# Kernel optimization log

Measured on AMD Instinct MI355X. Metric: run time of the kernel, lower is better.

The kernel has to match this reference:

```python
import jax, jax.numpy as jnp
import numpy as np

NC = 80
CENTER_RADIUS = 2.5
TOPK = 10
BOX_W, CLS_W, OBJ_W = 7.5, 0.5, 1.0
ALPHA, GAMMA = 0.25, 2.0
EPS = 1e-7
BIG = 1e10


def _corners(b):
    x, y, w, h = b[..., 0], b[..., 1], b[..., 2], b[..., 3]
    return x - w / 2, y - h / 2, x + w / 2, y + h / 2


def _pairwise_iou(b1, b2):
    # b1: (N,4) xywh, b2: (G,4) xywh -> (N,G) plain IoU
    x11, y11, x12, y12 = [t[:, None] for t in _corners(b1)]
    x21, y21, x22, y22 = _corners(b2)
    inter = jnp.clip(jnp.minimum(x12, x22) - jnp.maximum(x11, x21), 0) * \
            jnp.clip(jnp.minimum(y12, y22) - jnp.maximum(y11, y21), 0)
    union = (b1[:, 2] * b1[:, 3])[:, None] + (b2[:, 2] * b2[:, 3])[None, :] - inter + EPS
    return inter / union


def _ciou(b1, b2):
    # aligned boxes (N,4),(N,4) xywh -> (N,) CIoU
    x11, y11, x12, y12 = _corners(b1)
    x21, y21, x22, y22 = _corners(b2)
    w1, h1 = b1[..., 2], b1[..., 3]
    w2, h2 = b2[..., 2], b2[..., 3]
    inter = jnp.clip(jnp.minimum(x12, x22) - jnp.maximum(x11, x21), 0) * \
            jnp.clip(jnp.minimum(y12, y22) - jnp.maximum(y11, y21), 0)
    union = w1 * h1 + w2 * h2 - inter + EPS
    iou = inter / union
    cw = jnp.maximum(x12, x22) - jnp.minimum(x11, x21)
    ch = jnp.maximum(y12, y22) - jnp.minimum(y11, y21)
    c2 = cw ** 2 + ch ** 2 + EPS
    rho2 = ((x11 + x12 - x21 - x22) ** 2 + (y11 + y12 - y21 - y22) ** 2) / 4
    v = (4.0 / jnp.pi ** 2) * (jnp.arctan(w2 / (h2 + EPS)) - jnp.arctan(w1 / (h1 + EPS))) ** 2
    alpha = jax.lax.stop_gradient(v / (v - iou + (1.0 + EPS)))
    return iou - (rho2 / c2 + v * alpha)


def _assign(pred_boxes, pred_scores, gt_boxes, gt_classes, anchor_centers):
    # SimOTA: returns fg mask (N,) bool and matched gt index per anchor (N,)
    N = pred_boxes.shape[0]
    G = gt_boxes.shape[0]
    d = jnp.sqrt(jnp.sum((anchor_centers[:, None, :] - gt_boxes[None, :, :2]) ** 2, -1))
    cand = (d < CENTER_RADIUS).any(axis=1)                      # (N,) center prior
    cand = jnp.where(cand.any(), cand, jnp.ones_like(cand))     # fallback: all anchors
    n_cand = cand.sum().astype(jnp.int32)
    iou = _pairwise_iou(pred_boxes, gt_boxes)                   # (N,G)
    iou = jnp.where(cand[:, None], iou, 0.0)                    # candidates only
    iou_cost = -jnp.log(iou + 1e-8)
    # cls cost: BCE-with-logits of sigmoid scores vs one-hot gt, summed over classes.
    # sum_c bce(s_c, y_c) = sum_c softplus(s_c) - s_{gt}; avoids (N,G,nc) tensor.
    sp_sum = jax.nn.softplus(pred_scores).sum(axis=1)           # (N,)
    cls_cost = sp_sum[:, None] - pred_scores[:, gt_classes]     # (N,G)
    cost = jnp.where(cand[:, None], iou_cost + 3.0 * cls_cost, BIG)
    # dynamic-k: k_j = clip(floor(sum_i iou[i,j]), 1, min(topk, n_cand))
    dyn_k = jnp.maximum(jnp.floor(iou.sum(axis=0)).astype(jnp.int32), 1)
    dyn_k = jnp.minimum(dyn_k, jnp.minimum(TOPK, n_cand))       # (G,)
    _, topk_idx = jax.lax.top_k(-cost.T, TOPK)                  # (G,TOPK) smallest-cost anchors
    keep = jnp.arange(TOPK)[None, :] < dyn_k[:, None]           # (G,TOPK)
    matching = jnp.zeros((G, N), dtype=bool).at[jnp.arange(G)[:, None], topk_idx].set(keep)
    matching = matching.T                                       # (N,G)
    # conflict resolution: anchors matched to >1 gt keep only min-cost gt
    count = matching.sum(axis=1)
    best = jnp.argmin(jnp.where(matching, cost, BIG), axis=1)
    matching = jnp.where((count > 1)[:, None], jax.nn.one_hot(best, G, dtype=bool), matching)
    fg = matching.any(axis=1)
    matched_gt = jnp.argmax(matching, axis=1)
    return fg, matched_gt


def _image_loss(pred, gt_boxes, gt_classes, anchor_centers):
    pb = pred[:, :4]
    pc = pred[:, 4:4 + NC]
    po = pred[:, -1]
    fg, mgt = _assign(pb, jax.nn.sigmoid(pc), gt_boxes, gt_classes, anchor_centers)
    fg_f = fg.astype(pred.dtype)
    # objectness: BCE-with-logits, mean over anchors
    obj = (jax.nn.softplus(po) - po * fg_f).mean()
    # box: CIoU on matched pairs (masked sum)
    tgt_boxes = gt_boxes[mgt]                                   # (N,4)
    box = jnp.sum((1.0 - _ciou(pb, tgt_boxes)) * fg_f)
    # cls: focal BCE on matched anchors
    tgt_cls = jax.nn.one_hot(gt_classes[mgt], NC, dtype=pred.dtype)
    bce = jax.nn.softplus(pc) - pc * tgt_cls
    p = jax.nn.sigmoid(pc)
    p_t = p * tgt_cls + (1 - p) * (1 - tgt_cls)
    cls = jnp.sum((ALPHA * (1 - p_t) ** GAMMA * bce).sum(axis=1) * fg_f)
    return box, cls, obj, fg_f.sum()


def setup_inputs() -> dict:
    B, N, M = 4, 33600, 100
    key = jax.random.key(0)
    ks = jax.random.split(key, 7)
    boxes_xy = jax.random.uniform(ks[0], (B, N, 2)) * 640.0
    boxes_wh = jax.random.uniform(ks[1], (B, N, 2)) * 100.0 + 10.0
    logits = jax.random.normal(ks[2], (B, N, NC + 1))
    pred = jnp.concatenate([boxes_xy, boxes_wh, logits], axis=-1)    # (B,N,85)
    gt_xy = jax.random.uniform(ks[3], (B, M, 2)) * 640.0
    gt_wh = jax.random.uniform(ks[4], (B, M, 2)) * 100.0 + 10.0
    gt_boxes = jnp.concatenate([gt_xy, gt_wh], axis=-1)              # (B,M,4), all valid (sum>0)
    gt_classes = jax.random.randint(ks[5], (B, M), 0, NC, dtype=jnp.int32)
    anchor_centers = jax.random.uniform(ks[6], (N, 2)) * 640.0
    return {"pred": pred, "gt_boxes": gt_boxes, "gt_classes": gt_classes,
            "anchor_centers": anchor_centers}


def reference(pred, gt_boxes, gt_classes, anchor_centers):
    box, cls, obj, npos = jax.vmap(_image_loss, in_axes=(0, 0, 0, None))(
        pred, gt_boxes, gt_classes, anchor_centers)
    n_pos = jnp.maximum(npos.sum(), 1.0)
    total = BOX_W * box.sum() / n_pos + CLS_W * cls.sum() / n_pos + OBJ_W * obj.sum()
    return total
```

## Files before the change

kernel.cpp:

```cpp
#include <hip/hip_runtime.h>
#include <math.h>

#define B_ 4
#define N_ 33600
#define G_ 100
#define NCLS 80
#define STRIDE 85
#define TK 10
#define K1BLK 132
#define K3BLK 525
#define CAP 2048
#define PADW (K1BLK * 256)

__device__ __forceinline__ float sigmoidf_(float x) {
    return 1.0f / (1.0f + expf(-x));
}
__device__ __forceinline__ float softplusf_(float x) {
    return fmaxf(x, 0.0f) + log1pf(expf(-fabsf(x)));
}
__device__ __forceinline__ float waveRedSum(float v) {
    #pragma unroll
    for (int off = 32; off; off >>= 1) v += __shfl_xor(v, off, 64);
    return v;
}

__global__ void k1_prep(const float* __restrict__ gtb,
                        const float* __restrict__ anc,
                        const float* __restrict__ pred,
                        int* __restrict__ cidx_pad,
                        float* __restrict__ spsum,
                        unsigned long long* __restrict__ bkey,
                        float* __restrict__ pobj,
                        int* __restrict__ bcount,
                        unsigned int* __restrict__ done)
{
    __shared__ float gcx[G_], gcy[G_];
    __shared__ int wsum[4];
    __shared__ float wsf[4];
    const int b = blockIdx.y;
    const int tid = threadIdx.x;
    const int lane = tid & 63, wid = tid >> 6;
    if (blockIdx.x == 0 && b == 0 && tid == 0) *done = 0u;
    if (tid < G_) {
        gcx[tid] = gtb[(b * G_ + tid) * 4 + 0];
        gcy[tid] = gtb[(b * G_ + tid) * 4 + 1];
    }
    __syncthreads();
    const int n = blockIdx.x * blockDim.x + tid;
    float so = 0.0f;
    int c = 0;
    if (n < N_) {
        const size_t a_ = (size_t)b * N_ + n;
        bkey[a_] = 0xFFFFFFFFFFFFFFFFull;
        so = softplusf_(pred[a_ * STRIDE + (STRIDE - 1)]);
        const float2 a = ((const float2*)anc)[n];
        #pragma unroll 10
        for (int g = 0; g < G_; ++g) {
            const float dx = a.x - gcx[g], dy = a.y - gcy[g];
            c |= (dx * dx + dy * dy < 6.25f) ? 1 : 0;
        }
        unsigned long long m = __ballot(c != 0);
        while (m) {
            const int src = (int)__ffsll(m) - 1;
            m &= (m - 1);
            const int an = __shfl(n, src, 64);
            const float* row = pred + ((size_t)b * N_ + an) * STRIDE + 4;
            float s = softplusf_(sigmoidf_(row[lane]));
            if (lane < NCLS - 64) s += softplusf_(sigmoidf_(row[64 + lane]));
            s = waveRedSum(s);
            if (lane == 0) spsum[(size_t)b * N_ + an] = s;
        }
    }
    int incl = c;
    #pragma unroll
    for (int off = 1; off < 64; off <<= 1) {
        const int t = __shfl_up(incl, off, 64);
        if (lane >= off) incl += t;
    }
    if (lane == 63) wsum[wid] = incl;
    const float sow = waveRedSum(so);
    if (lane == 0) wsf[wid] = sow;
    __syncthreads();
    int wbase = 0;
    for (int w = 0; w < wid; ++w) wbase += wsum[w];
    if (c) cidx_pad[(size_t)b * PADW + blockIdx.x * 256 + wbase + incl - 1] = n;
    if (tid == 0) {
        pobj[b * K1BLK + blockIdx.x] = wsf[0] + wsf[1] + wsf[2] + wsf[3];
        bcount[b * K1BLK + blockIdx.x] = wsum[0] + wsum[1] + wsum[2] + wsum[3];
    }
}

__global__ void __launch_bounds__(256)
k2_topk(const float* __restrict__ pred,
        const float* __restrict__ gtb,
        const int* __restrict__ gtc,
        const int* __restrict__ cidx_pad,
        const int* __restrict__ bcount,
        const float* __restrict__ spsum,
        unsigned long long* __restrict__ bkey)
{
    const int b = blockIdx.y, g = blockIdx.x;
    const int tid = threadIdx.x;
    const int lane = tid & 63, wid = tid >> 6;

    __shared__ int scan[256];
    __shared__ int clds[CAP];
    __shared__ unsigned long long warr[4][TK];
    __shared__ float iolds[4];

    const int myc = (tid < K1BLK) ? bcount[b * K1BLK + tid] : 0;
    scan[tid] = myc;
    __syncthreads();
    #pragma unroll
    for (int off = 1; off < 256; off <<= 1) {
        const int v = (tid >= off) ? scan[tid - off] : 0;
        __syncthreads();
        scan[tid] += v;
        __syncthreads();
    }
    const int cnt = scan[K1BLK - 1];
    const int allc = (cnt == 0) ? 1 : 0;
    const int count = allc ? N_ : cnt;
    const int ebase = (tid == 0) ? 0 : scan[tid - 1];

    const float* gb = gtb + (b * G_ + g) * 4;
    const float gxc = gb[0], gyc = gb[1], gw = gb[2], gh = gb[3];
    const float gx1 = gxc - gw * 0.5f, gy1 = gyc - gh * 0.5f;
    const float gx2 = gxc + gw * 0.5f, gy2 = gyc + gh * 0.5f;
    const float garea = gw * gh;
    const int cls = gtc[b * G_ + g];

    float kcost[TK];
    int   kid[TK];
    #pragma unroll
    for (int j = 0; j < TK; ++j) { kcost[j] = INFINITY; kid[j] = 0x7FFFFFFF; }
    float iousum = 0.0f;

    for (int lo = 0; lo < count; lo += CAP) {
        const int hi = (count < lo + CAP) ? count : (lo + CAP);
        if (!allc && tid < K1BLK && myc) {
            for (int j = 0; j < myc; ++j) {
                const int d = ebase + j;
                if (d >= lo && d < hi)
                    clds[d - lo] = cidx_pad[(size_t)b * PADW + tid * 256 + j];
            }
        }
        __syncthreads();
        for (int i = lo + tid; i < hi; i += 256) {
            int n;
            float sp;
            if (allc) {
                n = i;
                const float* pr0 = pred + (size_t)(b * N_ + n) * STRIDE;
                float s = 0.0f;
                for (int cc = 0; cc < NCLS; ++cc) s += softplusf_(sigmoidf_(pr0[4 + cc]));
                sp = s;
            } else {
                n = clds[i - lo];
                sp = spsum[(size_t)b * N_ + n];
            }
            const float* pr = pred + (size_t)(b * N_ + n) * STRIDE;
            const float px = pr[0], py = pr[1], pw = pr[2], ph = pr[3];
            const float x1 = px - pw * 0.5f, y1 = py - ph * 0.5f;
            const float x2 = px + pw * 0.5f, y2 = py + ph * 0.5f;
            const float iw = fmaxf(fminf(x2, gx2) - fmaxf(x1, gx1), 0.0f);
            const float ih = fmaxf(fminf(y2, gy2) - fmaxf(y1, gy1), 0.0f);
            const float inter = iw * ih;
            const float uni = pw * ph + garea - inter + 1e-7f;
            const float iou = inter / uni;
            iousum += iou;
            const float sgc = sigmoidf_(pr[4 + cls]);
            float c = -logf(iou + 1e-8f) + 3.0f * (sp - sgc);
            int   s = n;
            #pragma unroll
            for (int j = 0; j < TK; ++j) {
                const bool lt = (c < kcost[j]);
                const float tc = kcost[j]; const int ts = kid[j];
                if (lt) { kcost[j] = c; kid[j] = s; c = tc; s = ts; }
            }
        }
        __syncthreads();
    }

    const float ios = waveRedSum(iousum);
    if (lane == 0) iolds[wid] = ios;

    #pragma unroll
    for (int r = 0; r < TK; ++r) {
        const unsigned long long mykey =
            ((unsigned long long)__float_as_uint(kcost[0]) << 32) | (unsigned)kid[0];
        unsigned long long k2 = mykey;
        #pragma unroll
        for (int off = 32; off; off >>= 1) {
            const unsigned long long o = __shfl_xor(k2, off, 64);
            k2 = (o < k2) ? o : k2;
        }
        if (lane == 0) warr[wid][r] = k2;
        if (mykey == k2) {
            #pragma unroll
            for (int j = 0; j < TK - 1; ++j) { kcost[j] = kcost[j + 1]; kid[j] = kid[j + 1]; }
            kcost[TK - 1] = INFINITY; kid[TK - 1] = 0x7FFFFFFF;
        }
    }
    __syncthreads();

    if (wid == 0) {
        unsigned long long key = 0xFFFFFFFFFFFFFFFFull;
        if (lane < 4 * TK) key = warr[lane / TK][lane % TK];
        unsigned long long win[TK];
        #pragma unroll
        for (int r = 0; r < TK; ++r) {
            unsigned long long k2 = key;
            #pragma unroll
            for (int off = 32; off; off >>= 1) {
                const unsigned long long o = __shfl_xor(k2, off, 64);
                k2 = (o < k2) ? o : k2;
            }
            win[r] = k2;
            if (key == k2) key = 0xFFFFFFFFFFFFFFFFull;
        }
        const float total_iou = iolds[0] + iolds[1] + iolds[2] + iolds[3];
        const int kmax = (count < TK) ? count : TK;
        int dk = (int)floorf(total_iou);
        if (dk < 1) dk = 1;
        if (dk > kmax) dk = kmax;
        if (lane == 0) {
            #pragma unroll
            for (int r = 0; r < TK; ++r) {
                if (r < dk) {
                    const int n = (int)(unsigned)(win[r] & 0xFFFFFFFFull);
                    const unsigned cbits = (unsigned)(win[r] >> 32);
                    const unsigned long long key2 =
                        ((unsigned long long)cbits << 32) | (unsigned)g;
                    atomicMin(&bkey[(size_t)b * N_ + n], key2);
                }
            }
        }
    }
}

__global__ void k3_fg(const float* __restrict__ pred,
                      const float* __restrict__ gtb,
                      const int* __restrict__ gtc,
                      const unsigned long long* __restrict__ bkey,
                      const float* __restrict__ pobj,
                      float* __restrict__ pfg,
                      unsigned int* __restrict__ done,
                      float* __restrict__ out)
{
    const int tid = threadIdx.x;
    const unsigned i = blockIdx.x * blockDim.x + tid;
    const int lane = tid & 63, wid = tid >> 6;
    const unsigned long long key = bkey[i];
    const bool fg = (key != 0xFFFFFFFFFFFFFFFFull);
    float posum = 0.0f, box = 0.0f, clsacc = 0.0f, npos = 0.0f;

    unsigned long long m = __ballot(fg);
    while (m) {
        const int src = (int)__ffsll(m) - 1;
        m &= (m - 1);
        const unsigned ai = (unsigned)__shfl((int)i, src, 64);
        const int mg = __shfl((int)(unsigned)(key & 0xFFFFFFFFull), src, 64);
        const int b = (int)(ai / (unsigned)N_);
        const float* pr = pred + (size_t)ai * STRIDE;
        const int cg_ = gtc[b * G_ + mg];
        {
            const float x = pr[4 + lane];
            const float t = (lane == cg_) ? 1.0f : 0.0f;
            const float bce = softplusf_(x) - x * t;
            const float p = sigmoidf_(x);
            const float pt = t * p + (1.0f - t) * (1.0f - p);
            const float om = 1.0f - pt;
            clsacc += 0.25f * om * om * bce;
        }
        if (lane < NCLS - 64) {
            const float x = pr[4 + 64 + lane];
            const float t = ((64 + lane) == cg_) ? 1.0f : 0.0f;
            const float bce = softplusf_(x) - x * t;
            const float p = sigmoidf_(x);
            const float pt = t * p + (1.0f - t) * (1.0f - p);
            const float om = 1.0f - pt;
            clsacc += 0.25f * om * om * bce;
        }
        if (lane == 0) {
            npos += 1.0f;
            posum += pr[STRIDE - 1];
            const float* gb = gtb + (b * G_ + mg) * 4;
            const float px = pr[0], py = pr[1], pw = pr[2], ph = pr[3];
            const float gx = gb[0], gy = gb[1], gw = gb[2], gh = gb[3];
            const float x11 = px - pw * 0.5f, y11 = py - ph * 0.5f;
            const float x12 = px + pw * 0.5f, y12 = py + ph * 0.5f;
            const float x21 = gx - gw * 0.5f, y21 = gy - gh * 0.5f;
            const float x22 = gx + gw * 0.5f, y22 = gy + gh * 0.5f;
            const float iw = fmaxf(fminf(x12, x22) - fmaxf(x11, x21), 0.0f);
            const float ih = fmaxf(fminf(y12, y22) - fmaxf(y11, y21), 0.0f);
            const float inter = iw * ih;
            const float uni = pw * ph + gw * gh - inter + 1e-7f;
            const float iou = inter / uni;
            const float cw = fmaxf(x12, x22) - fminf(x11, x21);
            const float chh = fmaxf(y12, y22) - fminf(y11, y21);
            const float c2 = cw * cw + chh * chh + 1e-7f;
            const float ddx = x11 + x12 - x21 - x22;
            const float ddy = y11 + y12 - y21 - y22;
            const float rho2 = (ddx * ddx + ddy * ddy) * 0.25f;
            const float dv = atanf(gw / (gh + 1e-7f)) - atanf(pw / (ph + 1e-7f));
            const float v = (float)(4.0 / (M_PI * M_PI)) * dv * dv;
            const float alpha = v / (v - iou + 1.0f + 1e-7f);
            const float ciou = iou - (rho2 / c2 + v * alpha);
            box += 1.0f - ciou;
        }
    }

    posum = waveRedSum(posum);
    box = waveRedSum(box);
    clsacc = waveRedSum(clsacc);
    npos = waveRedSum(npos);
    __shared__ float ws[4][4];
    if (lane == 0) {
        ws[wid][0] = posum; ws[wid][1] = box;
        ws[wid][2] = clsacc; ws[wid][3] = npos;
    }
    __syncthreads();
    __shared__ int amlast;
    if (tid == 0) {
        float* p = pfg + (size_t)blockIdx.x * 4;
        #pragma unroll
        for (int k = 0; k < 4; ++k) {
            const float v = ws[0][k] + ws[1][k] + ws[2][k] + ws[3][k];
            __hip_atomic_store(&p[k], v, __ATOMIC_RELAXED, __HIP_MEMORY_SCOPE_AGENT);
        }
        const unsigned prev = __hip_atomic_fetch_add(done, 1u, __ATOMIC_ACQ_REL,
                                                     __HIP_MEMORY_SCOPE_AGENT);
        amlast = (prev == (unsigned)(K3BLK - 1)) ? 1 : 0;
    }
    __syncthreads();
    if (!amlast) return;

    float so = 0, sp = 0, sb = 0, sc = 0, sn = 0;
    for (int k = tid; k < B_ * K1BLK; k += 256) so += pobj[k];
    for (int k = tid; k < K3BLK; k += 256) {
        const float* p = pfg + (size_t)k * 4;
        sp += __hip_atomic_load(&p[0], __ATOMIC_RELAXED, __HIP_MEMORY_SCOPE_AGENT);
        sb += __hip_atomic_load(&p[1], __ATOMIC_RELAXED, __HIP_MEMORY_SCOPE_AGENT);
        sc += __hip_atomic_load(&p[2], __ATOMIC_RELAXED, __HIP_MEMORY_SCOPE_AGENT);
        sn += __hip_atomic_load(&p[3], __ATOMIC_RELAXED, __HIP_MEMORY_SCOPE_AGENT);
    }
    __shared__ float red[256];
    float in5[5] = {so, sp, sb, sc, sn};
    float res[5];
    #pragma unroll
    for (int k = 0; k < 5; ++k) {
        red[tid] = in5[k];
        __syncthreads();
        for (int s = 128; s > 0; s >>= 1) {
            if (tid < s) red[tid] += red[tid + s];
            __syncthreads();
        }
        res[k] = red[0];
        __syncthreads();
    }
    if (tid == 0) {
        const float obj_sum = res[0] - res[1];
        const float n_pos = fmaxf(res[4], 1.0f);
        out[0] = 7.5f * res[2] / n_pos
               + 0.5f * res[3] / n_pos
               + obj_sum / (float)N_;
    }
}

extern "C" void kernel_launch(void* const* d_in, const int* in_sizes, int n_in,
                              void* d_out, int out_size, void* d_ws, size_t ws_size,
                              hipStream_t stream)
{
    const float* pred = (const float*)d_in[0];
    const float* gtb  = (const float*)d_in[1];
    const int*   gtc  = (const int*)d_in[2];
    const float* anc  = (const float*)d_in[3];

    char* ws = (char*)d_ws;
    size_t off = 0;
    auto take = [&](size_t bytes) {
        size_t o = off;
        off += (bytes + 255) & ~(size_t)255;
        return o;
    };
    int*                cidx_pad = (int*)(ws + take((size_t)B_ * PADW * 4));
    unsigned long long* bkey     = (unsigned long long*)(ws + take((size_t)B_ * N_ * 8));
    float*              spsum    = (float*)(ws + take((size_t)B_ * N_ * 4));
    float*              pobj     = (float*)(ws + take((size_t)B_ * K1BLK * 4));
    int*                bcount   = (int*)(ws + take((size_t)B_ * K1BLK * 4));
    float*              pfg      = (float*)(ws + take((size_t)K3BLK * 4 * 4));
    unsigned int*       done     = (unsigned int*)(ws + take(4));

    dim3 g1(K1BLK, B_);
    k1_prep<<<g1, 256, 0, stream>>>(gtb, anc, pred, cidx_pad, spsum, bkey,
                                    pobj, bcount, done);
    dim3 g2(G_, B_);
    k2_topk<<<g2, 256, 0, stream>>>(pred, gtb, gtc, cidx_pad, bcount, spsum, bkey);
    k3_fg<<<K3BLK, 256, 0, stream>>>(pred, gtb, gtc, bkey, pobj, pfg, done,
                                     (float*)d_out);
}
```

Before: 41.52 us.

## Fuse foreground loss into top-k assignment kernel via atomicMin delta accounting

```diff
diff --git a/kernel.cpp b/kernel.cpp
--- a/kernel.cpp
+++ b/kernel.cpp
@@ -8,7 +8,7 @@
 #define STRIDE 85
 #define TK 10
 #define K1BLK 132
-#define K3BLK 525
+#define K2TOT (B_ * G_)
 #define CAP 2048
 #define PADW (K1BLK * 256)
 
@@ -32,6 +32,7 @@
                         unsigned long long* __restrict__ bkey,
                         float* __restrict__ pobj,
                         int* __restrict__ bcount,
+                        float* __restrict__ acc,
                         unsigned int* __restrict__ done)
 {
     __shared__ float gcx[G_], gcy[G_];
@@ -40,7 +41,10 @@
     const int b = blockIdx.y;
     const int tid = threadIdx.x;
     const int lane = tid & 63, wid = tid >> 6;
-    if (blockIdx.x == 0 && b == 0 && tid == 0) *done = 0u;
+    if (blockIdx.x == 0 && b == 0 && tid == 0) {
+        *done = 0u;
+        acc[0] = 0.0f; acc[1] = 0.0f; acc[2] = 0.0f; acc[3] = 0.0f;
+    }
     if (tid < G_) {
         gcx[tid] = gtb[(b * G_ + tid) * 4 + 0];
         gcy[tid] = gtb[(b * G_ + tid) * 4 + 1];
@@ -90,14 +94,78 @@
     }
 }
 
+struct Contrib { float cls, box, po; };
+__device__ __noinline__ Contrib contribEval(const float* __restrict__ pred,
+                                            const float* __restrict__ gtb,
+                                            const int* __restrict__ gtc,
+                                            int b, int n, int gg, int lane)
+{
+    Contrib c;
+    const float* pr = pred + (size_t)(b * N_ + n) * STRIDE;
+    const int cg_ = gtc[b * G_ + gg];
+    float cl;
+    {
+        const float x = pr[4 + lane];
+        const float t = (lane == cg_) ? 1.0f : 0.0f;
+        const float bce = softplusf_(x) - x * t;
+        const float p = sigmoidf_(x);
+        const float pt = t * p + (1.0f - t) * (1.0f - p);
+        const float om = 1.0f - pt;
+        cl = 0.25f * om * om * bce;
+    }
+    if (lane < NCLS - 64) {
+        const float x = pr[4 + 64 + lane];
+        const float t = ((64 + lane) == cg_) ? 1.0f : 0.0f;
+        const float bce = softplusf_(x) - x * t;
+        const float p = sigmoidf_(x);
+        const float pt = t * p + (1.0f - t) * (1.0f - p);
+        const float om = 1.0f - pt;
+        cl += 0.25f * om * om * bce;
+    }
+    c.cls = cl;
+    c.box = 0.0f;
+    c.po = 0.0f;
+    if (lane == 0) {
+        c.po = pr[STRIDE - 1];
+        const float* gb = gtb + (b * G_ + gg) * 4;
+        const float px = pr[0], py = pr[1], pw = pr[2], ph = pr[3];
+        const float gx = gb[0], gy = gb[1], gw = gb[2], gh = gb[3];
+        const float x11 = px - pw * 0.5f, y11 = py - ph * 0.5f;
+        const float x12 = px + pw * 0.5f, y12 = py + ph * 0.5f;
+        const float x21 = gx - gw * 0.5f, y21 = gy - gh * 0.5f;
+        const float x22 = gx + gw * 0.5f, y22 = gy + gh * 0.5f;
+        const float iw = fmaxf(fminf(x12, x22) - fmaxf(x11, x21), 0.0f);
+        const float ih = fmaxf(fminf(y12, y22) - fmaxf(y11, y21), 0.0f);
+        const float inter = iw * ih;
+        const float uni = pw * ph + gw * gh - inter + 1e-7f;
+        const float iou = inter / uni;
+        const float cw = fmaxf(x12, x22) - fminf(x11, x21);
+        const float chh = fmaxf(y12, y22) - fminf(y11, y21);
+        const float c2 = cw * cw + chh * chh + 1e-7f;
+        const float ddx = x11 + x12 - x21 - x22;
+        const float ddy = y11 + y12 - y21 - y22;
+        const float rho2 = (ddx * ddx + ddy * ddy) * 0.25f;
+        const float dv = atanf(gw / (gh + 1e-7f)) - atanf(pw / (ph + 1e-7f));
+        const float v = (float)(4.0 / (M_PI * M_PI)) * dv * dv;
+        const float alpha = v / (v - iou + 1.0f + 1e-7f);
+        const float ciou = iou - (rho2 / c2 + v * alpha);
+        c.box = 1.0f - ciou;
+    }
+    return c;
+}
+
 __global__ void __launch_bounds__(256)
-k2_topk(const float* __restrict__ pred,
-        const float* __restrict__ gtb,
-        const int* __restrict__ gtc,
-        const int* __restrict__ cidx_pad,
-        const int* __restrict__ bcount,
-        const float* __restrict__ spsum,
-        unsigned long long* __restrict__ bkey)
+k2_assign(const float* __restrict__ pred,
+          const float* __restrict__ gtb,
+          const int* __restrict__ gtc,
+          const int* __restrict__ cidx_pad,
+          const int* __restrict__ bcount,
+          const float* __restrict__ spsum,
+          unsigned long long* __restrict__ bkey,
+          const float* __restrict__ pobj,
+          float* __restrict__ acc,
+          unsigned int* __restrict__ done,
+          float* __restrict__ out)
 {
     const int b = blockIdx.y, g = blockIdx.x;
     const int tid = threadIdx.x;
@@ -107,6 +175,8 @@
     __shared__ int clds[CAP];
     __shared__ unsigned long long warr[4][TK];
     __shared__ float iolds[4];
+    __shared__ unsigned long long swin[TK];
+    __shared__ int sdk;
 
     const int myc = (tid < K1BLK) ? bcount[b * K1BLK + tid] : 0;
     scan[tid] = myc;
@@ -207,7 +277,6 @@
     if (wid == 0) {
         unsigned long long key = 0xFFFFFFFFFFFFFFFFull;
         if (lane < 4 * TK) key = warr[lane / TK][lane % TK];
-        unsigned long long win[TK];
         #pragma unroll
         for (int r = 0; r < TK; ++r) {
             unsigned long long k2 = key;
@@ -216,98 +285,40 @@
                 const unsigned long long o = __shfl_xor(k2, off, 64);
                 k2 = (o < k2) ? o : k2;
             }
-            win[r] = k2;
+            if (lane == 0) swin[r] = k2;
             if (key == k2) key = 0xFFFFFFFFFFFFFFFFull;
         }
-        const float total_iou = iolds[0] + iolds[1] + iolds[2] + iolds[3];
-        const int kmax = (count < TK) ? count : TK;
-        int dk = (int)floorf(total_iou);
-        if (dk < 1) dk = 1;
-        if (dk > kmax) dk = kmax;
         if (lane == 0) {
-            #pragma unroll
-            for (int r = 0; r < TK; ++r) {
-                if (r < dk) {
-                    const int n = (int)(unsigned)(win[r] & 0xFFFFFFFFull);
-                    const unsigned cbits = (unsigned)(win[r] >> 32);
-                    const unsigned long long key2 =
-                        ((unsigned long long)cbits << 32) | (unsigned)g;
-                    atomicMin(&bkey[(size_t)b * N_ + n], key2);
-                }
+            const float total_iou = iolds[0] + iolds[1] + iolds[2] + iolds[3];
+            const int kmax = (count < TK) ? count : TK;
+            int dk = (int)floorf(total_iou);
+            if (dk < 1) dk = 1;
+            if (dk > kmax) dk = kmax;
+            sdk = dk;
+        }
+    }
+    __syncthreads();
+
+    float clsacc = 0.0f, box = 0.0f, posum = 0.0f, npos = 0.0f;
+    const int dk = sdk;
+    for (int r = wid; r < dk; r += 4) {
+        const unsigned long long w = swin[r];
+        const int n = (int)(unsigned)(w & 0xFFFFFFFFull);
+        const unsigned long long mykey =
+            (w & 0xFFFFFFFF00000000ull) | (unsigned)g;
+        unsigned long long old = 0;
+        if (lane == 0) old = atomicMin(&bkey[(size_t)b * N_ + n], mykey);
+        old = __shfl(old, 0, 64);
+        if (mykey < old) {
+            const Contrib ca = contribEval(pred, gtb, gtc, b, n, g, lane);
+            clsacc += ca.cls; box += ca.box; posum += ca.po;
+            if (lane == 0) npos += 1.0f;
+            if (old != 0xFFFFFFFFFFFFFFFFull) {
+                const int og = (int)(unsigned)(old & 0xFFFFFFFFull);
+                const Contrib cs = contribEval(pred, gtb, gtc, b, n, og, lane);
+                clsacc -= cs.cls; box -= cs.box; posum -= cs.po;
+                if (lane == 0) npos -= 1.0f;
             }
-        }
-    }
-}
-
-__global__ void k3_fg(const float* __restrict__ pred,
-                      const float* __restrict__ gtb,
-                      const int* __restrict__ gtc,
-                      const unsigned long long* __restrict__ bkey,
-                      const float* __restrict__ pobj,
-                      float* __restrict__ pfg,
-                      unsigned int* __restrict__ done,
-                      float* __restrict__ out)
-{
-    const int tid = threadIdx.x;
-    const unsigned i = blockIdx.x * blockDim.x + tid;
-    const int lane = tid & 63, wid = tid >> 6;
-    const unsigned long long key = bkey[i];
-    const bool fg = (key != 0xFFFFFFFFFFFFFFFFull);
-    float posum = 0.0f, box = 0.0f, clsacc = 0.0f, npos = 0.0f;
-
-    unsigned long long m = __ballot(fg);
-    while (m) {
-        const int src = (int)__ffsll(m) - 1;
-        m &= (m - 1);
-        const unsigned ai = (unsigned)__shfl((int)i, src, 64);
-        const int mg = __shfl((int)(unsigned)(key & 0xFFFFFFFFull), src, 64);
-        const int b = (int)(ai / (unsigned)N_);
-        const float* pr = pred + (size_t)ai * STRIDE;
-        const int cg_ = gtc[b * G_ + mg];
-        {
-            const float x = pr[4 + lane];
-            const float t = (lane == cg_) ? 1.0f : 0.0f;
-            const float bce = softplusf_(x) - x * t;
-            const float p = sigmoidf_(x);
-            const float pt = t * p + (1.0f - t) * (1.0f - p);
-            const float om = 1.0f - pt;
-            clsacc += 0.25f * om * om * bce;
-        }
-        if (lane < NCLS - 64) {
-            const float x = pr[4 + 64 + lane];
-            const float t = ((64 + lane) == cg_) ? 1.0f : 0.0f;
-            const float bce = softplusf_(x) - x * t;
-            const float p = sigmoidf_(x);
-            const float pt = t * p + (1.0f - t) * (1.0f - p);
-            const float om = 1.0f - pt;
-            clsacc += 0.25f * om * om * bce;
-        }
-        if (lane == 0) {
-            npos += 1.0f;
-            posum += pr[STRIDE - 1];
-            const float* gb = gtb + (b * G_ + mg) * 4;
-            const float px = pr[0], py = pr[1], pw = pr[2], ph = pr[3];
-            const float gx = gb[0], gy = gb[1], gw = gb[2], gh = gb[3];
-            const float x11 = px - pw * 0.5f, y11 = py - ph * 0.5f;
-            const float x12 = px + pw * 0.5f, y12 = py + ph * 0.5f;
-            const float x21 = gx - gw * 0.5f, y21 = gy - gh * 0.5f;
-            const float x22 = gx + gw * 0.5f, y22 = gy + gh * 0.5f;
-            const float iw = fmaxf(fminf(x12, x22) - fmaxf(x11, x21), 0.0f);
-            const float ih = fmaxf(fminf(y12, y22) - fmaxf(y11, y21), 0.0f);
-            const float inter = iw * ih;
-            const float uni = pw * ph + gw * gh - inter + 1e-7f;
-            const float iou = inter / uni;
-            const float cw = fmaxf(x12, x22) - fminf(x11, x21);
-            const float chh = fmaxf(y12, y22) - fminf(y11, y21);
-            const float c2 = cw * cw + chh * chh + 1e-7f;
-            const float ddx = x11 + x12 - x21 - x22;
-            const float ddy = y11 + y12 - y21 - y22;
-            const float rho2 = (ddx * ddx + ddy * ddy) * 0.25f;
-            const float dv = atanf(gw / (gh + 1e-7f)) - atanf(pw / (ph + 1e-7f));
-            const float v = (float)(4.0 / (M_PI * M_PI)) * dv * dv;
-            const float alpha = v / (v - iou + 1.0f + 1e-7f);
-            const float ciou = iou - (rho2 / c2 + v * alpha);
-            box += 1.0f - ciou;
         }
     }
 
@@ -315,56 +326,47 @@
     box = waveRedSum(box);
     clsacc = waveRedSum(clsacc);
     npos = waveRedSum(npos);
-    __shared__ float ws[4][4];
+    __shared__ float ws4[4][4];
     if (lane == 0) {
-        ws[wid][0] = posum; ws[wid][1] = box;
-        ws[wid][2] = clsacc; ws[wid][3] = npos;
+        ws4[wid][0] = posum; ws4[wid][1] = box;
+        ws4[wid][2] = clsacc; ws4[wid][3] = npos;
     }
     __syncthreads();
     __shared__ int amlast;
     if (tid == 0) {
-        float* p = pfg + (size_t)blockIdx.x * 4;
-        #pragma unroll
-        for (int k = 0; k < 4; ++k) {
-            const float v = ws[0][k] + ws[1][k] + ws[2][k] + ws[3][k];
-            __hip_atomic_store(&p[k], v, __ATOMIC_RELAXED, __HIP_MEMORY_SCOPE_AGENT);
-        }
+        const float r0 = ws4[0][0] + ws4[1][0] + ws4[2][0] + ws4[3][0];
+        const float r1 = ws4[0][1] + ws4[1][1] + ws4[2][1] + ws4[3][1];
+        const float r2 = ws4[0][2] + ws4[1][2] + ws4[2][2] + ws4[3][2];
+        const float r3 = ws4[0][3] + ws4[1][3] + ws4[2][3] + ws4[3][3];
+        atomicAdd(&acc[0], r0);
+        atomicAdd(&acc[1], r1);
+        atomicAdd(&acc[2], r2);
+        atomicAdd(&acc[3], r3);
         const unsigned prev = __hip_atomic_fetch_add(done, 1u, __ATOMIC_ACQ_REL,
                                                      __HIP_MEMORY_SCOPE_AGENT);
-        amlast = (prev == (unsigned)(K3BLK - 1)) ? 1 : 0;
+        amlast = (prev == (unsigned)(K2TOT - 1)) ? 1 : 0;
     }
     __syncthreads();
     if (!amlast) return;
 
-    float so = 0, sp = 0, sb = 0, sc = 0, sn = 0;
+    float so = 0.0f;
     for (int k = tid; k < B_ * K1BLK; k += 256) so += pobj[k];
-    for (int k = tid; k < K3BLK; k += 256) {
-        const float* p = pfg + (size_t)k * 4;
-        sp += __hip_atomic_load(&p[0], __ATOMIC_RELAXED, __HIP_MEMORY_SCOPE_AGENT);
-        sb += __hip_atomic_load(&p[1], __ATOMIC_RELAXED, __HIP_MEMORY_SCOPE_AGENT);
-        sc += __hip_atomic_load(&p[2], __ATOMIC_RELAXED, __HIP_MEMORY_SCOPE_AGENT);
-        sn += __hip_atomic_load(&p[3], __ATOMIC_RELAXED, __HIP_MEMORY_SCOPE_AGENT);
-    }
     __shared__ float red[256];
-    float in5[5] = {so, sp, sb, sc, sn};
-    float res[5];
-    #pragma unroll
-    for (int k = 0; k < 5; ++k) {
-        red[tid] = in5[k];
+    red[tid] = so;
+    __syncthreads();
+    for (int s = 128; s > 0; s >>= 1) {
+        if (tid < s) red[tid] += red[tid + s];
         __syncthreads();
-        for (int s = 128; s > 0; s >>= 1) {
-            if (tid < s) red[tid] += red[tid + s];
-            __syncthreads();
-        }
-        res[k] = red[0];
-        __syncthreads();
     }
     if (tid == 0) {
-        const float obj_sum = res[0] - res[1];
-        const float n_pos = fmaxf(res[4], 1.0f);
-        out[0] = 7.5f * res[2] / n_pos
-               + 0.5f * res[3] / n_pos
-               + obj_sum / (float)N_;
+        const float posumT = __hip_atomic_load(&acc[0], __ATOMIC_RELAXED, __HIP_MEMORY_SCOPE_AGENT);
+        const float boxT   = __hip_atomic_load(&acc[1], __ATOMIC_RELAXED, __HIP_MEMORY_SCOPE_AGENT);
+        const float clsT   = __hip_atomic_load(&acc[2], __ATOMIC_RELAXED, __HIP_MEMORY_SCOPE_AGENT);
+        const float nposT  = __hip_atomic_load(&acc[3], __ATOMIC_RELAXED, __HIP_MEMORY_SCOPE_AGENT);
+        const float n_pos = fmaxf(nposT, 1.0f);
+        out[0] = 7.5f * boxT / n_pos
+               + 0.5f * clsT / n_pos
+               + (red[0] - posumT) / (float)N_;
     }
 }
 
@@ -389,14 +391,13 @@
     float*              spsum    = (float*)(ws + take((size_t)B_ * N_ * 4));
     float*              pobj     = (float*)(ws + take((size_t)B_ * K1BLK * 4));
     int*                bcount   = (int*)(ws + take((size_t)B_ * K1BLK * 4));
-    float*              pfg      = (float*)(ws + take((size_t)K3BLK * 4 * 4));
+    float*              acc      = (float*)(ws + take(4 * 4));
     unsigned int*       done     = (unsigned int*)(ws + take(4));
 
     dim3 g1(K1BLK, B_);
     k1_prep<<<g1, 256, 0, stream>>>(gtb, anc, pred, cidx_pad, spsum, bkey,
-                                    pobj, bcount, done);
+                                    pobj, bcount, acc, done);
     dim3 g2(G_, B_);
-    k2_topk<<<g2, 256, 0, stream>>>(pred, gtb, gtc, cidx_pad, bcount, spsum, bkey);
-    k3_fg<<<K3BLK, 256, 0, stream>>>(pred, gtb, gtc, bkey, pobj, pfg, done,
-                                     (float*)d_out);
-}
+    k2_assign<<<g2, 256, 0, stream>>>(pred, gtb, gtc, cidx_pad, bcount, spsum,
+                                      bkey, pobj, acc, done, (float*)d_out);
+}
```

After: 49.88 us. 1.2x slower.
